# Performance work log

Hardware: AMD Instinct MI355X
Metric: run time of the kernel (lower is better)

Reference implementation:

```python
import jax, jax.numpy as jnp
import numpy as np
from jax import lax

B, T, D, H, L, OUT = 4, 1024, 1024, 16, 6, 1024
DH = D // H


def _ln(x, g, b, eps=1e-5):
    mu = jnp.mean(x, axis=-1, keepdims=True)
    var = jnp.mean(jnp.square(x - mu), axis=-1, keepdims=True)
    return (x - mu) * lax.rsqrt(var + eps) * g + b


def setup_inputs() -> dict:
    key = jax.random.key(0)
    ks = iter(jax.random.split(key, 32))
    s = 0.02
    inp = {
        "seq": jax.random.normal(next(ks), (B, T, D), jnp.float32),
        "pos_emb": jax.random.normal(next(ks), (1, T, D), jnp.float32) * s,
        # per-layer params stacked on leading L axis; linear weights stored [in, out]
        "ln1_g": jnp.ones((L, D), jnp.float32),
        "ln1_b": jnp.zeros((L, D), jnp.float32),
        "wq": jax.random.normal(next(ks), (L, D, D), jnp.float32) * s,
        "bq": jnp.zeros((L, D), jnp.float32),
        "wk": jax.random.normal(next(ks), (L, D, D), jnp.float32) * s,
        "bk": jnp.zeros((L, D), jnp.float32),
        "wv": jax.random.normal(next(ks), (L, D, D), jnp.float32) * s,
        "bv": jnp.zeros((L, D), jnp.float32),
        "wo": jax.random.normal(next(ks), (L, D, D), jnp.float32) * s,
        "bo": jnp.zeros((L, D), jnp.float32),
        "ln2_g": jnp.ones((L, D), jnp.float32),
        "ln2_b": jnp.zeros((L, D), jnp.float32),
        "w1": jax.random.normal(next(ks), (L, D, 4 * D), jnp.float32) * s,
        "b1": jnp.zeros((L, 4 * D), jnp.float32),
        "w2": jax.random.normal(next(ks), (L, 4 * D, D), jnp.float32) * s,
        "b2": jnp.zeros((L, D), jnp.float32),
        "lnf_g": jnp.ones((D,), jnp.float32),
        "lnf_b": jnp.zeros((D,), jnp.float32),
        "w_head": jax.random.normal(next(ks), (D, OUT), jnp.float32) * s,
    }
    return inp


def _gpt(seq, pos_emb, ln1_g, ln1_b, wq, bq, wk, bk, wv, bv, wo, bo,
         ln2_g, ln2_b, w1, b1, w2, b2, lnf_g, lnf_b, w_head):
    x = seq + pos_emb  # embedding dropout is identity in eval

    def block(x, p):
        (g1, b1g, Wq, Bq, Wk, Bk, Wv, Bv, Wo, Bo, g2, b2g, W1, B1, W2, B2) = p
        h = _ln(x, g1, b1g)
        q = (h @ Wq + Bq).reshape(B, T, H, DH)
        k = (h @ Wk + Bk).reshape(B, T, H, DH)
        v = (h @ Wv + Bv).reshape(B, T, H, DH)
        # NOTE: original mask buffer is all ones -> no causal masking (faithful)
        att = jnp.einsum('bthd,bshd->bhts', q, k) * (1.0 / np.sqrt(DH))
        att = jax.nn.softmax(att, axis=-1)
        y = jnp.einsum('bhts,bshd->bthd', att, v).reshape(B, T, D)
        x = x + (y @ Wo + Bo)
        h2 = _ln(x, g2, b2g)
        x = x + (jax.nn.gelu(h2 @ W1 + B1, approximate=False) @ W2 + B2)
        return x, None

    params = (ln1_g, ln1_b, wq, bq, wk, bk, wv, bv, wo, bo,
              ln2_g, ln2_b, w1, b1, w2, b2)
    x, _ = lax.scan(block, x, params)
    x = _ln(x, lnf_g, lnf_b)
    return x @ w_head


def reference(seq, pos_emb, ln1_g, ln1_b, wq, bq, wk, bk, wv, bv, wo, bo,
              ln2_g, ln2_b, w1, b1, w2, b2, lnf_g, lnf_b, w_head):
    return _gpt(seq, pos_emb, ln1_g, ln1_b, wq, bq, wk, bk, wv, bv, wo, bo,
                ln2_g, ln2_b, w1, b1, w2, b2, lnf_g, lnf_b, w_head)
```

## Files before the change

kernel.cpp:

```cpp
#include <hip/hip_runtime.h>
#include <math.h>

#define BB 4
#define TT 1024
#define DD 1024
#define HH 16
#define LL 6
#define DHH 64
#define MM (BB*TT)
#define QKVLD 3072

typedef short bf16x8 __attribute__((ext_vector_type(8)));
typedef float floatx4 __attribute__((ext_vector_type(4)));

#define AS1 __attribute__((address_space(1)))
#define AS3 __attribute__((address_space(3)))

__device__ __forceinline__ void g2l16(const void* g, void* l) {
    __builtin_amdgcn_global_load_lds((const AS1 unsigned int*)g,
                                     (AS3 unsigned int*)l, 16, 0, 0);
}

__device__ __forceinline__ unsigned short f2bf(float f) {
    unsigned u = __builtin_bit_cast(unsigned, f);
    u += 0x7fffu + ((u >> 16) & 1u);
    return (unsigned short)(u >> 16);
}

__global__ __launch_bounds__(256) void add_pos_kernel(
    const float* __restrict__ seq, const float* __restrict__ pos, float* __restrict__ x)
{
    int i = blockIdx.x * 256 + threadIdx.x;
    const int TD4 = TT * DD / 4;
    float4 s = ((const float4*)seq)[i];
    float4 p = ((const float4*)pos)[i & (TD4 - 1)];
    ((float4*)x)[i] = make_float4(s.x + p.x, s.y + p.y, s.z + p.z, s.w + p.w);
}

__global__ __launch_bounds__(256) void concat_bias_kernel(
    const float* __restrict__ bq, const float* __restrict__ bk,
    const float* __restrict__ bv, float* __restrict__ bqkv)
{
    int i = blockIdx.x * 256 + threadIdx.x;
    int l = i / QKVLD, j = i - l * QKVLD;
    float v;
    if (j < DD)            v = bq[l*DD + j];
    else if (j < 2*DD)     v = bk[l*DD + j - DD];
    else                   v = bv[l*DD + j - 2*DD];
    bqkv[i] = v;
}

__global__ __launch_bounds__(256) void ln_kernel(
    const float* __restrict__ x, const float* __restrict__ g,
    const float* __restrict__ b, unsigned short* __restrict__ out)
{
    __shared__ float red[8];
    int row = blockIdx.x;
    int tid = threadIdx.x;
    const float4* xr = (const float4*)(x + (size_t)row * DD);
    float4 v = xr[tid];
    float s  = v.x + v.y + v.z + v.w;
    float ss = v.x*v.x + v.y*v.y + v.z*v.z + v.w*v.w;
    #pragma unroll
    for (int o = 32; o > 0; o >>= 1) {
        s  += __shfl_down(s,  o, 64);
        ss += __shfl_down(ss, o, 64);
    }
    int wid = tid >> 6, lid = tid & 63;
    if (lid == 0) { red[wid] = s; red[4 + wid] = ss; }
    __syncthreads();
    float sum  = red[0] + red[1] + red[2] + red[3];
    float sums = red[4] + red[5] + red[6] + red[7];
    float mean = sum * (1.0f / DD);
    float var  = sums * (1.0f / DD) - mean * mean;
    float inv  = rsqrtf(var + 1e-5f);
    float4 gg = ((const float4*)g)[tid];
    float4 bb = ((const float4*)b)[tid];
    ushort4 o4;
    o4.x = f2bf((v.x - mean) * inv * gg.x + bb.x);
    o4.y = f2bf((v.y - mean) * inv * gg.y + bb.y);
    o4.z = f2bf((v.z - mean) * inv * gg.z + bb.z);
    o4.w = f2bf((v.w - mean) * inv * gg.w + bb.w);
    ((ushort4*)(out + (size_t)row * DD))[tid] = o4;
}

__global__ __launch_bounds__(256) void transpose_bf16(
    const float* __restrict__ W, unsigned short* __restrict__ Wt, int K, int N)
{
    __shared__ float tile[32][33];
    int n0 = blockIdx.x * 32, k0 = blockIdx.y * 32;
    int tx = threadIdx.x & 31, ty = threadIdx.x >> 5;
    #pragma unroll
    for (int i = 0; i < 4; i++)
        tile[ty + i*8][tx] = W[(size_t)(k0 + ty + i*8) * N + n0 + tx];
    __syncthreads();
    #pragma unroll
    for (int i = 0; i < 4; i++)
        Wt[(size_t)(n0 + ty + i*8) * K + k0 + tx] = f2bf(tile[tx][ty + i*8]);
}

template<int ACT, int RES, int OUTBF>
__global__ __launch_bounds__(256) void mfma_gemm(
    const unsigned short* __restrict__ A, const unsigned short* __restrict__ Bt,
    const float* __restrict__ bias, const float* __restrict__ res,
    void* __restrict__ Cv, int M, int N, int K)
{
    __shared__ unsigned short As0[128*32], As1[128*32];
    __shared__ unsigned short Bs0[128*32], Bs1[128*32];
    const int tid = threadIdx.x;
    const int wave = tid >> 6, lane = tid & 63;
    const int quad = lane >> 4, lc = lane & 15;

    const int bid = blockIdx.x;
    const int xcd = bid & 7;
    const int j = bid >> 3;
    const int m0 = (xcd * 4 + (j & 3)) << 7;
    const int n0 = (j >> 2) << 7;

    const unsigned short* Ag = A  + (size_t)(m0 + wave*32 + (lane>>2)) * K + (lane&3)*8;
    const unsigned short* Bg = Bt + (size_t)(n0 + wave*32 + (lane>>2)) * K + (lane&3)*8;
    unsigned short* Al0 = &As0[wave*32*32];
    unsigned short* Bl0 = &Bs0[wave*32*32];
    unsigned short* Al1 = &As1[wave*32*32];
    unsigned short* Bl1 = &Bs1[wave*32*32];

    const int wm = (wave & 1) * 64, wn = (wave >> 1) * 64;

    floatx4 acc[4][4];
    #pragma unroll
    for (int i = 0; i < 4; i++)
        #pragma unroll
        for (int jj = 0; jj < 4; jj++) acc[i][jj] = (floatx4)0.0f;

    for (int k0 = 0; k0 < K; k0 += 64) {
        __syncthreads();
        g2l16(Ag + k0,                     Al0);
        g2l16(Ag + k0 + (size_t)16*K,      Al0 + 16*32);
        g2l16(Bg + k0,                     Bl0);
        g2l16(Bg + k0 + (size_t)16*K,      Bl0 + 16*32);
        g2l16(Ag + k0 + 32,                Al1);
        g2l16(Ag + k0 + 32 + (size_t)16*K, Al1 + 16*32);
        g2l16(Bg + k0 + 32,                Bl1);
        g2l16(Bg + k0 + 32 + (size_t)16*K, Bl1 + 16*32);
        __syncthreads();
        #pragma unroll
        for (int hh = 0; hh < 2; hh++) {
            const unsigned short* Asx = hh ? As1 : As0;
            const unsigned short* Bsx = hh ? Bs1 : Bs0;
            bf16x8 af[4], bf[4];
            #pragma unroll
            for (int i = 0; i < 4; i++)
                af[i] = *(const bf16x8*)&Asx[(wm + i*16 + lc)*32 + quad*8];
            #pragma unroll
            for (int jj = 0; jj < 4; jj++)
                bf[jj] = *(const bf16x8*)&Bsx[(wn + jj*16 + lc)*32 + quad*8];
            #pragma unroll
            for (int i = 0; i < 4; i++)
                #pragma unroll
                for (int jj = 0; jj < 4; jj++)
                    acc[i][jj] = __builtin_amdgcn_mfma_f32_16x16x32_bf16(af[i], bf[jj], acc[i][jj], 0, 0, 0);
        }
    }

    #pragma unroll
    for (int jj = 0; jj < 4; jj++) {
        int n = n0 + wn + jj*16 + lc;
        float bv = bias ? bias[n] : 0.0f;
        #pragma unroll
        for (int i = 0; i < 4; i++) {
            int mbase = m0 + wm + i*16 + quad*4;
            #pragma unroll
            for (int r = 0; r < 4; r++) {
                int m = mbase + r;
                float v = acc[i][jj][r] + bv;
                if (ACT) v = 0.5f * v * (1.0f + erff(v * 0.70710678118654752f));
                if (RES) v += res[(size_t)m * N + n];
                if (OUTBF) ((unsigned short*)Cv)[(size_t)m * N + n] = f2bf(v);
                else       ((float*)Cv)[(size_t)m * N + n] = v;
            }
        }
    }
}

#define LSTR 88
__global__ __launch_bounds__(256) void attn_mfma(
    const unsigned short* __restrict__ qkv, unsigned short* __restrict__ y)
{
    __shared__ unsigned short Qs[64*LSTR];
    __shared__ unsigned short Ks[64*LSTR];
    __shared__ unsigned short Ps[64*LSTR];
    const int tid = threadIdx.x, wave = tid >> 6, lane = tid & 63;
    const int quad = lane >> 4, lc = lane & 15;
    const int t0 = blockIdx.x * 64;
    const int b = blockIdx.y >> 4, h = blockIdx.y & 15;

    const unsigned short* q = qkv;
    const unsigned short* k = qkv + DD;
    const unsigned short* v = qkv + 2*DD;

    const size_t rowbase = (size_t)b * TT;
    const int sr = tid >> 2, sc = (tid & 3) * 16;

    {
        const unsigned short* src = q + (rowbase + t0 + sr) * QKVLD + h*DHH + sc;
        *(uint4*)&Qs[sr*LSTR + sc]     = *(const uint4*)src;
        *(uint4*)&Qs[sr*LSTR + sc + 8] = *(const uint4*)(src + 8);
    }

    float m_r[4], l_r[4];
    floatx4 o_acc[4];
    #pragma unroll
    for (int r = 0; r < 4; r++) { m_r[r] = -1e30f; l_r[r] = 0.0f; }
    #pragma unroll
    for (int f = 0; f < 4; f++) o_acc[f] = (floatx4)0.0f;

    for (int s0 = 0; s0 < TT; s0 += 64) {
        __syncthreads();
        {
            const unsigned short* src = k + (rowbase + s0 + sr) * QKVLD + h*DHH + sc;
            *(uint4*)&Ks[sr*LSTR + sc]     = *(const uint4*)src;
            *(uint4*)&Ks[sr*LSTR + sc + 8] = *(const uint4*)(src + 8);
        }
        __syncthreads();

        floatx4 s[4];
        #pragma unroll
        for (int f = 0; f < 4; f++) s[f] = (floatx4)0.0f;
        #pragma unroll
        for (int c = 0; c < 2; c++) {
            bf16x8 aq = *(const bf16x8*)&Qs[(wave*16 + lc)*LSTR + c*32 + quad*8];
            #pragma unroll
            for (int f = 0; f < 4; f++) {
                bf16x8 bk = *(const bf16x8*)&Ks[(f*16 + lc)*LSTR + c*32 + quad*8];
                s[f] = __builtin_amdgcn_mfma_f32_16x16x32_bf16(aq, bk, s[f], 0, 0, 0);
            }
        }

        #pragma unroll
        for (int r = 0; r < 4; r++) {
            float mt = fmaxf(fmaxf(s[0][r], s[1][r]), fmaxf(s[2][r], s[3][r])) * 0.125f;
            #pragma unroll
            for (int d = 1; d < 16; d <<= 1) mt = fmaxf(mt, __shfl_xor(mt, d, 64));
            float mn = fmaxf(m_r[r], mt);
            float alpha = __expf(m_r[r] - mn);
            m_r[r] = mn;
            float rs = 0.0f;
            #pragma unroll
            for (int f = 0; f < 4; f++) {
                float p = __expf(s[f][r] * 0.125f - mn);
                s[f][r] = p;
                rs += p;
            }
            #pragma unroll
            for (int d = 1; d < 16; d <<= 1) rs += __shfl_xor(rs, d, 64);
            l_r[r] = l_r[r] * alpha + rs;
            #pragma unroll
            for (int f = 0; f < 4; f++) o_acc[f][r] *= alpha;
        }

        #pragma unroll
        for (int f = 0; f < 4; f++)
            #pragma unroll
            for (int r = 0; r < 4; r++)
                Ps[(wave*16 + quad*4 + r)*LSTR + f*16 + lc] = f2bf(s[f][r]);

        __syncthreads();
        {
            const unsigned short* src = v + (rowbase + s0 + sr) * QKVLD + h*DHH + sc;
            uint4 v0 = *(const uint4*)src;
            uint4 v1 = *(const uint4*)(src + 8);
            unsigned short tmp[16];
            *(uint4*)&tmp[0] = v0;
            *(uint4*)&tmp[8] = v1;
            #pragma unroll
            for (int e = 0; e < 16; e++)
                Ks[(sc + e)*LSTR + sr] = tmp[e];
        }
        __syncthreads();

        #pragma unroll
        for (int c = 0; c < 2; c++) {
            bf16x8 ap = *(const bf16x8*)&Ps[(wave*16 + lc)*LSTR + c*32 + quad*8];
            #pragma unroll
            for (int f = 0; f < 4; f++) {
                bf16x8 bv = *(const bf16x8*)&Ks[(f*16 + lc)*LSTR + c*32 + quad*8];
                o_acc[f] = __builtin_amdgcn_mfma_f32_16x16x32_bf16(ap, bv, o_acc[f], 0, 0, 0);
            }
        }
    }

    unsigned short* yg = y + (rowbase + t0) * DD + h*DHH;
    #pragma unroll
    for (int f = 0; f < 4; f++)
        #pragma unroll
        for (int r = 0; r < 4; r++)
            yg[(size_t)(wave*16 + quad*4 + r) * DD + f*16 + lc] = f2bf(o_acc[f][r] / l_r[r]);
}

extern "C" void kernel_launch(void* const* d_in, const int* in_sizes, int n_in,
                              void* d_out, int out_size, void* d_ws, size_t ws_size,
                              hipStream_t stream)
{
    const float* seq    = (const float*)d_in[0];
    const float* pos    = (const float*)d_in[1];
    const float* ln1_g  = (const float*)d_in[2];
    const float* ln1_b  = (const float*)d_in[3];
    const float* wq     = (const float*)d_in[4];
    const float* bq     = (const float*)d_in[5];
    const float* wk     = (const float*)d_in[6];
    const float* bk     = (const float*)d_in[7];
    const float* wv     = (const float*)d_in[8];
    const float* bv     = (const float*)d_in[9];
    const float* wo     = (const float*)d_in[10];
    const float* bo     = (const float*)d_in[11];
    const float* ln2_g  = (const float*)d_in[12];
    const float* ln2_b  = (const float*)d_in[13];
    const float* w1     = (const float*)d_in[14];
    const float* b1     = (const float*)d_in[15];
    const float* w2     = (const float*)d_in[16];
    const float* b2     = (const float*)d_in[17];
    const float* lnf_g  = (const float*)d_in[18];
    const float* lnf_b  = (const float*)d_in[19];
    const float* w_head = (const float*)d_in[20];
    float* out = (float*)d_out;

    const size_t MSZ = (size_t)MM * DD;
    float* x            = (float*)d_ws;
    unsigned short* h   = (unsigned short*)(x + MSZ);
    unsigned short* qkv = h + MSZ;
    unsigned short* ub  = qkv + (size_t)MM * QKVLD;
    unsigned short* wt  = ub + (size_t)MM * 4 * DD;
    unsigned short* wtq = wt;
    unsigned short* wtk = wt + (size_t)DD*DD;
    unsigned short* wtv = wt + (size_t)2*DD*DD;
    unsigned short* wto = wt + (size_t)3*DD*DD;
    unsigned short* wt1 = wt + (size_t)4*DD*DD;
    unsigned short* wt2 = wt + (size_t)8*DD*DD;
    float* bqkv         = (float*)(wt + (size_t)12*DD*DD);

    dim3 blk(256);
    dim3 g1(32*8);
    dim3 gq(32*24);
    dim3 g4(32*32);
    dim3 tsq(32, 32);
    dim3 t14(128, 32);
    dim3 t41(32, 128);
    dim3 ag(16, 64);

    add_pos_kernel<<<4096, blk, 0, stream>>>(seq, pos, x);
    concat_bias_kernel<<<LL*QKVLD/256, blk, 0, stream>>>(bq, bk, bv, bqkv);

    for (int l = 0; l < LL; l++) {
        const size_t wofs  = (size_t)l * DD * DD;
        const size_t bofs  = (size_t)l * DD;
        const size_t w1ofs = (size_t)l * DD * 4 * DD;
        const size_t b1ofs = (size_t)l * 4 * DD;

        transpose_bf16<<<tsq, blk, 0, stream>>>(wq + wofs, wtq, DD, DD);
        transpose_bf16<<<tsq, blk, 0, stream>>>(wk + wofs, wtk, DD, DD);
        transpose_bf16<<<tsq, blk, 0, stream>>>(wv + wofs, wtv, DD, DD);
        transpose_bf16<<<tsq, blk, 0, stream>>>(wo + wofs, wto, DD, DD);
        transpose_bf16<<<t14, blk, 0, stream>>>(w1 + w1ofs, wt1, DD, 4*DD);
        transpose_bf16<<<t41, blk, 0, stream>>>(w2 + w1ofs, wt2, 4*DD, DD);

        ln_kernel<<<MM, blk, 0, stream>>>(x, ln1_g + bofs, ln1_b + bofs, h);
        mfma_gemm<0,0,1><<<gq, blk, 0, stream>>>(h, wt, bqkv + (size_t)l*QKVLD, nullptr, qkv, MM, QKVLD, DD);
        attn_mfma<<<ag, blk, 0, stream>>>(qkv, h);
        mfma_gemm<0,1,0><<<g1, blk, 0, stream>>>(h, wto, bo + bofs, x, x, MM, DD, DD);
        ln_kernel<<<MM, blk, 0, stream>>>(x, ln2_g + bofs, ln2_b + bofs, h);
        mfma_gemm<1,0,1><<<g4, blk, 0, stream>>>(h, wt1, b1 + b1ofs, nullptr, ub, MM, 4*DD, DD);
        mfma_gemm<0,1,0><<<g1, blk, 0, stream>>>(ub, wt2, b2 + bofs, x, x, MM, DD, 4*DD);
    }

    ln_kernel<<<MM, blk, 0, stream>>>(x, lnf_g, lnf_b, h);
    transpose_bf16<<<tsq, blk, 0, stream>>>(w_head, wtq, DD, DD);
    mfma_gemm<0,0,0><<<g1, blk, 0, stream>>>(h, wtq, nullptr, nullptr, out, MM, DD, DD);
}
```

Measured before the change: 2.193 ms.

## Register-prefetch double-buffered GEMM and merge per-layer weight transposes into one launch

The GEMM main loop moves from direct global-to-LDS loads of a 64-wide K slab, with two barriers per iteration, to register prefetch of the next 32-wide K slab into a double-buffered LDS tile with one barrier per iteration. The intent is to overlap global loads with MFMA work. The cost is extra VGPRs and twice as many loop iterations. Separately, the six per-layer weight transpose launches are merged into a single launch to reduce launch overhead.

```diff
diff --git a/kernel.cpp b/kernel.cpp
--- a/kernel.cpp
+++ b/kernel.cpp
@@ -12,14 +12,6 @@
 
 typedef short bf16x8 __attribute__((ext_vector_type(8)));
 typedef float floatx4 __attribute__((ext_vector_type(4)));
-
-#define AS1 __attribute__((address_space(1)))
-#define AS3 __attribute__((address_space(3)))
-
-__device__ __forceinline__ void g2l16(const void* g, void* l) {
-    __builtin_amdgcn_global_load_lds((const AS1 unsigned int*)g,
-                                     (AS3 unsigned int*)l, 16, 0, 0);
-}
 
 __device__ __forceinline__ unsigned short f2bf(float f) {
     unsigned u = __builtin_bit_cast(unsigned, f);
@@ -84,6 +76,40 @@
     ((ushort4*)(out + (size_t)row * DD))[tid] = o4;
 }
 
+__global__ __launch_bounds__(256) void transpose_layer(
+    const float* __restrict__ wq, const float* __restrict__ wk,
+    const float* __restrict__ wv, const float* __restrict__ wo,
+    const float* __restrict__ w1, const float* __restrict__ w2,
+    unsigned short* __restrict__ wt)
+{
+    __shared__ float tile[32][33];
+    const size_t DD2 = (size_t)DD * DD;
+    int bid = blockIdx.x;
+    const float* src; unsigned short* dst; int K, N, n0, k0;
+    if (bid < 4096) {
+        int r = bid >> 10, t = bid & 1023;
+        src = (r == 0) ? wq : (r == 1) ? wk : (r == 2) ? wv : wo;
+        dst = wt + (size_t)r * DD2; K = DD; N = DD;
+        n0 = (t & 31) * 32; k0 = (t >> 5) * 32;
+    } else if (bid < 8192) {
+        int t = bid - 4096;
+        src = w1; dst = wt + 4 * DD2; K = DD; N = 4 * DD;
+        n0 = (t & 127) * 32; k0 = (t >> 7) * 32;
+    } else {
+        int t = bid - 8192;
+        src = w2; dst = wt + 8 * DD2; K = 4 * DD; N = DD;
+        n0 = (t & 31) * 32; k0 = (t >> 5) * 32;
+    }
+    int tx = threadIdx.x & 31, ty = threadIdx.x >> 5;
+    #pragma unroll
+    for (int i = 0; i < 4; i++)
+        tile[ty + i*8][tx] = src[(size_t)(k0 + ty + i*8) * N + n0 + tx];
+    __syncthreads();
+    #pragma unroll
+    for (int i = 0; i < 4; i++)
+        dst[(size_t)(n0 + ty + i*8) * K + k0 + tx] = f2bf(tile[tx][ty + i*8]);
+}
+
 __global__ __launch_bounds__(256) void transpose_bf16(
     const float* __restrict__ W, unsigned short* __restrict__ Wt, int K, int N)
 {
@@ -105,8 +131,8 @@
     const float* __restrict__ bias, const float* __restrict__ res,
     void* __restrict__ Cv, int M, int N, int K)
 {
-    __shared__ unsigned short As0[128*32], As1[128*32];
-    __shared__ unsigned short Bs0[128*32], Bs1[128*32];
+    __shared__ unsigned short As[2][128*32];
+    __shared__ unsigned short Bs[2][128*32];
     const int tid = threadIdx.x;
     const int wave = tid >> 6, lane = tid & 63;
     const int quad = lane >> 4, lc = lane & 15;
@@ -117,12 +143,10 @@
     const int m0 = (xcd * 4 + (j & 3)) << 7;
     const int n0 = (j >> 2) << 7;
 
-    const unsigned short* Ag = A  + (size_t)(m0 + wave*32 + (lane>>2)) * K + (lane&3)*8;
-    const unsigned short* Bg = Bt + (size_t)(n0 + wave*32 + (lane>>2)) * K + (lane&3)*8;
-    unsigned short* Al0 = &As0[wave*32*32];
-    unsigned short* Bl0 = &Bs0[wave*32*32];
-    unsigned short* Al1 = &As1[wave*32*32];
-    unsigned short* Bl1 = &Bs1[wave*32*32];
+    const int srow = tid >> 2, scol = (tid & 3) * 8;
+    const unsigned short* Ag = A  + (size_t)(m0 + srow) * K + scol;
+    const unsigned short* Bg = Bt + (size_t)(n0 + srow) * K + scol;
+    const int lds_lo = srow * 32 + scol, lds_hi = (64 + srow) * 32 + scol;
 
     const int wm = (wave & 1) * 64, wn = (wave >> 1) * 64;
 
@@ -132,34 +156,37 @@
         #pragma unroll
         for (int jj = 0; jj < 4; jj++) acc[i][jj] = (floatx4)0.0f;
 
-    for (int k0 = 0; k0 < K; k0 += 64) {
-        __syncthreads();
-        g2l16(Ag + k0,                     Al0);
-        g2l16(Ag + k0 + (size_t)16*K,      Al0 + 16*32);
-        g2l16(Bg + k0,                     Bl0);
-        g2l16(Bg + k0 + (size_t)16*K,      Bl0 + 16*32);
-        g2l16(Ag + k0 + 32,                Al1);
-        g2l16(Ag + k0 + 32 + (size_t)16*K, Al1 + 16*32);
-        g2l16(Bg + k0 + 32,                Bl1);
-        g2l16(Bg + k0 + 32 + (size_t)16*K, Bl1 + 16*32);
-        __syncthreads();
-        #pragma unroll
-        for (int hh = 0; hh < 2; hh++) {
-            const unsigned short* Asx = hh ? As1 : As0;
-            const unsigned short* Bsx = hh ? Bs1 : Bs0;
-            bf16x8 af[4], bf[4];
-            #pragma unroll
-            for (int i = 0; i < 4; i++)
-                af[i] = *(const bf16x8*)&Asx[(wm + i*16 + lc)*32 + quad*8];
+    uint4 pa0 = *(const uint4*)(Ag);
+    uint4 pa1 = *(const uint4*)(Ag + (size_t)64 * K);
+    uint4 pb0 = *(const uint4*)(Bg);
+    uint4 pb1 = *(const uint4*)(Bg + (size_t)64 * K);
+
+    int cur = 0;
+    for (int k0 = 0; k0 < K; k0 += 32) {
+        *(uint4*)&As[cur][lds_lo] = pa0;
+        *(uint4*)&As[cur][lds_hi] = pa1;
+        *(uint4*)&Bs[cur][lds_lo] = pb0;
+        *(uint4*)&Bs[cur][lds_hi] = pb1;
+        __syncthreads();
+        if (k0 + 32 < K) {
+            pa0 = *(const uint4*)(Ag + k0 + 32);
+            pa1 = *(const uint4*)(Ag + k0 + 32 + (size_t)64 * K);
+            pb0 = *(const uint4*)(Bg + k0 + 32);
+            pb1 = *(const uint4*)(Bg + k0 + 32 + (size_t)64 * K);
+        }
+        bf16x8 af[4], bfr[4];
+        #pragma unroll
+        for (int i = 0; i < 4; i++)
+            af[i] = *(const bf16x8*)&As[cur][(wm + i*16 + lc)*32 + quad*8];
+        #pragma unroll
+        for (int jj = 0; jj < 4; jj++)
+            bfr[jj] = *(const bf16x8*)&Bs[cur][(wn + jj*16 + lc)*32 + quad*8];
+        #pragma unroll
+        for (int i = 0; i < 4; i++)
             #pragma unroll
             for (int jj = 0; jj < 4; jj++)
-                bf[jj] = *(const bf16x8*)&Bsx[(wn + jj*16 + lc)*32 + quad*8];
-            #pragma unroll
-            for (int i = 0; i < 4; i++)
-                #pragma unroll
-                for (int jj = 0; jj < 4; jj++)
-                    acc[i][jj] = __builtin_amdgcn_mfma_f32_16x16x32_bf16(af[i], bf[jj], acc[i][jj], 0, 0, 0);
-        }
+                acc[i][jj] = __builtin_amdgcn_mfma_f32_16x16x32_bf16(af[i], bfr[jj], acc[i][jj], 0, 0, 0);
+        cur ^= 1;
     }
 
     #pragma unroll
@@ -330,9 +357,6 @@
     unsigned short* qkv = h + MSZ;
     unsigned short* ub  = qkv + (size_t)MM * QKVLD;
     unsigned short* wt  = ub + (size_t)MM * 4 * DD;
-    unsigned short* wtq = wt;
-    unsigned short* wtk = wt + (size_t)DD*DD;
-    unsigned short* wtv = wt + (size_t)2*DD*DD;
     unsigned short* wto = wt + (size_t)3*DD*DD;
     unsigned short* wt1 = wt + (size_t)4*DD*DD;
     unsigned short* wt2 = wt + (size_t)8*DD*DD;
@@ -343,8 +367,6 @@
     dim3 gq(32*24);
     dim3 g4(32*32);
     dim3 tsq(32, 32);
-    dim3 t14(128, 32);
-    dim3 t41(32, 128);
     dim3 ag(16, 64);
 
     add_pos_kernel<<<4096, blk, 0, stream>>>(seq, pos, x);
@@ -356,12 +378,8 @@
         const size_t w1ofs = (size_t)l * DD * 4 * DD;
         const size_t b1ofs = (size_t)l * 4 * DD;
 
-        transpose_bf16<<<tsq, blk, 0, stream>>>(wq + wofs, wtq, DD, DD);
-        transpose_bf16<<<tsq, blk, 0, stream>>>(wk + wofs, wtk, DD, DD);
-        transpose_bf16<<<tsq, blk, 0, stream>>>(wv + wofs, wtv, DD, DD);
-        transpose_bf16<<<tsq, blk, 0, stream>>>(wo + wofs, wto, DD, DD);
-        transpose_bf16<<<t14, blk, 0, stream>>>(w1 + w1ofs, wt1, DD, 4*DD);
-        transpose_bf16<<<t41, blk, 0, stream>>>(w2 + w1ofs, wt2, 4*DD, DD);
+        transpose_layer<<<12288, blk, 0, stream>>>(
+            wq + wofs, wk + wofs, wv + wofs, wo + wofs, w1 + w1ofs, w2 + w1ofs, wt);
 
         ln_kernel<<<MM, blk, 0, stream>>>(x, ln1_g + bofs, ln1_b + bofs, h);
         mfma_gemm<0,0,1><<<gq, blk, 0, stream>>>(h, wt, bqkv + (size_t)l*QKVLD, nullptr, qkv, MM, QKVLD, DD);
@@ -373,6 +391,6 @@
     }
 
     ln_kernel<<<MM, blk, 0, stream>>>(x, lnf_g, lnf_b, h);
-    transpose_bf16<<<tsq, blk, 0, stream>>>(w_head, wtq, DD, DD);
-    mfma_gemm<0,0,0><<<g1, blk, 0, stream>>>(h, wtq, nullptr, nullptr, out, MM, DD, DD);
-}
+    transpose_bf16<<<tsq, blk, 0, stream>>>(w_head, wt, DD, DD);
+    mfma_gemm<0,0,0><<<g1, blk, 0, stream>>>(h, wt, nullptr, nullptr, out, MM, DD, DD);
+}
```

New measurement: 2.004 ms. -8.6%, faster.
